# Performance work log

Hardware: AMD Instinct MI355X
Metric: run time of the kernel (lower is better)

Reference implementation:

```python
import jax, jax.numpy as jnp
import numpy as np

QB = 127.0  # 8-bit activation quant range
EPS = 1e-5


def _bitlinear(x, w, b):
    # BitNet b1.58-style BitLinear.
    # Activation: per-token absmax 8-bit quantization (STE).
    s = QB / jnp.clip(jnp.max(jnp.abs(x), axis=-1, keepdims=True), EPS)
    xq = jnp.clip(jnp.round(x * s), -QB - 1.0, QB) / s
    xq = x + jax.lax.stop_gradient(xq - x)
    # Weight: ternary {-1,0,1} with absmean scaling (STE).
    ws = 1.0 / jnp.clip(jnp.mean(jnp.abs(w)), EPS)
    wq = jnp.clip(jnp.round(w * ws), -1.0, 1.0) / ws
    wq = w + jax.lax.stop_gradient(wq - w)
    return jnp.einsum('bsf,of->bso', xq, wq) + b


def setup_inputs() -> dict:
    key = jax.random.key(0)
    k1, k2, k3, k4, k5, k6 = jax.random.split(key, 6)
    B, S, F = 8, 32768, 128
    evidence = jax.random.normal(k1, (B, S, F), dtype=jnp.float32)
    prior_belief = jax.random.uniform(k2, (B, S, F), dtype=jnp.float32)
    # belief_update params: Linear(2F -> F), Linear(F -> F)
    W1 = jax.random.normal(k3, (F, 2 * F), dtype=jnp.float32) * (1.0 / np.sqrt(2 * F))
    b1 = jax.random.normal(k4, (F,), dtype=jnp.float32) * 0.01
    W2 = jax.random.normal(k5, (F, F), dtype=jnp.float32) * (1.0 / np.sqrt(F))
    b2 = jax.random.normal(k6, (F,), dtype=jnp.float32) * 0.01
    return {"evidence": evidence, "prior_belief": prior_belief,
            "W1": W1, "b1": b1, "W2": W2, "b2": b2}


def reference(evidence, prior_belief, W1, b1, W2, b2):
    # update network: BitLinear -> ReLU -> BitLinear -> Sigmoid
    upd_in = jnp.concatenate([prior_belief, evidence], axis=-1)  # [B,S,2F]
    h = jax.nn.relu(_bitlinear(upd_in, W1, b1))                  # [B,S,F]
    likelihood = jax.nn.sigmoid(_bitlinear(h, W2, b2))           # [B,S,F]
    posterior_unnorm = prior_belief * likelihood
    normalizer = jnp.clip(posterior_unnorm.sum(axis=1, keepdims=True), 1e-10)
    return posterior_unnorm / normalizer
```

## Files before the change

### kernel.cpp

```cpp
#include <hip/hip_runtime.h>
#include <hip/hip_bf16.h>
#include <math.h>

typedef int   i32x4 __attribute__((ext_vector_type(4)));
typedef unsigned int u32;

#define QBF 127.0f
#define EPSF 1e-5f
#define FF 128
#define NROWS (8 * 32768)
#define NBLK 512
#define TPB 8

#define W2_OFF    32768
#define WBUF_OFF  49152
#define CS_OFF    66560
#define LDS_TOTAL 68608

#define WB() __builtin_amdgcn_wave_barrier()

static __device__ __forceinline__ float bcast_lane(float v, int lane) {
    return __builtin_bit_cast(float, __builtin_amdgcn_readlane(__builtin_bit_cast(int, v), lane));
}
static __device__ __forceinline__ u32 packi8(float a, float b, float c, float d, float s) {
    int i0 = (int)rintf(a * s), i1 = (int)rintf(b * s);
    int i2 = (int)rintf(c * s), i3 = (int)rintf(d * s);
    return (u32)(i0 & 0xFF) | ((u32)(i1 & 0xFF) << 8) |
           ((u32)(i2 & 0xFF) << 16) | ((u32)i3 << 24);
}

__global__ void wstats_kernel(const float* __restrict__ W1,
                              const float* __restrict__ W2,
                              float* __restrict__ hdr) {
    __shared__ double red[1024];
    int t = threadIdx.x;
    double s = 0.0;
    #pragma unroll
    for (int i = 0; i < 8; ++i) {
        float4 v = *(const float4*)(W1 + (i * 1024 + t) * 4);
        s += (double)fabsf(v.x) + (double)fabsf(v.y)
           + (double)fabsf(v.z) + (double)fabsf(v.w);
    }
    red[t] = s; __syncthreads();
    for (int o = 512; o > 0; o >>= 1) { if (t < o) red[t] += red[t + o]; __syncthreads(); }
    if (t == 0) hdr[0] = 1.0f / fmaxf((float)(red[0] * (1.0 / 32768.0)), EPSF);
    __syncthreads();
    s = 0.0;
    #pragma unroll
    for (int i = 0; i < 4; ++i) {
        float4 v = *(const float4*)(W2 + (i * 1024 + t) * 4);
        s += (double)fabsf(v.x) + (double)fabsf(v.y)
           + (double)fabsf(v.z) + (double)fabsf(v.w);
    }
    red[t] = s; __syncthreads();
    for (int o = 512; o > 0; o >>= 1) { if (t < o) red[t] += red[t + o]; __syncthreads(); }
    if (t == 0) hdr[1] = 1.0f / fmaxf((float)(red[0] * (1.0 / 16384.0)), EPSF);
}

__global__ void wquant_kernel(const float* __restrict__ W1,
                              const float* __restrict__ W2,
                              const float* __restrict__ hdr,
                              char* __restrict__ wq) {
    int g = blockIdx.x * 256 + threadIdx.x;
    float ws1 = hdr[0], ws2 = hdr[1];
    const float* src; float wsx; char* dst;
    if (g < 2048) {
        int gi = g >> 6, l = g & 63;
        int ct = gi >> 2, kb = gi & 3;
        src = W1 + (ct * 16 + (l & 15)) * 256 + kb * 64 + (l >> 4) * 16;
        wsx = ws1;
        dst = wq + gi * 1024 + l * 16;
    } else {
        int g2 = g - 2048;
        int gi = g2 >> 6, l = g2 & 63;
        int ct = gi >> 1, kb = gi & 1;
        src = W2 + (ct * 16 + (l & 15)) * 128 + kb * 64 + (l >> 4) * 16;
        wsx = ws2;
        dst = wq + 32768 + gi * 1024 + l * 16;
    }
    u32 o[4];
    #pragma unroll
    for (int q = 0; q < 4; ++q) {
        float4 v = *(const float4*)(src + q * 4);
        float q0 = fminf(fmaxf(rintf(v.x * wsx), -1.f), 1.f);
        float q1 = fminf(fmaxf(rintf(v.y * wsx), -1.f), 1.f);
        float q2 = fminf(fmaxf(rintf(v.z * wsx), -1.f), 1.f);
        float q3 = fminf(fmaxf(rintf(v.w * wsx), -1.f), 1.f);
        o[q] = packi8(q0, q1, q2, q3, 1.0f);
    }
    *(uint4*)dst = make_uint4(o[0], o[1], o[2], o[3]);
}

__global__ __launch_bounds__(256, 2) void fused_kernel(
    const float* __restrict__ evid, const float* __restrict__ prior,
    const float* __restrict__ bias1, const float* __restrict__ bias2,
    const char* __restrict__ wq, const float* __restrict__ hdr,
    float* __restrict__ out, float* __restrict__ partials)
{
    __shared__ __align__(16) char smem[LDS_TOTAL];
    const int tid = threadIdx.x;
    const int w = tid >> 6, l = tid & 63;
    const int lr = l & 15, lg = l >> 4;
    const int lc = l & 31, half = l >> 5;
    char* wbuf = smem + WBUF_OFF + w * 4352;
    float* colsum = (float*)(smem + CS_OFF);
    const float ws1 = hdr[0], ws2 = hdr[1];

    {
        const uint4* g = (const uint4*)wq;
        #pragma unroll
        for (int i = 0; i < 12; ++i) {
            uint4 v = g[i * 256 + tid];
            *(uint4*)(smem + (size_t)(i * 256 + tid) * 16) = v;
        }
    }
    float4 xr[16];
    {
        const float* srcp = half ? evid : prior;
        int R0 = blockIdx.x * 512 + w * 16;
        #pragma unroll
        for (int r = 0; r < 16; ++r)
            xr[r] = *(const float4*)(srcp + (size_t)(R0 + r) * FF + lc * 4);
    }
    __syncthreads();

    float4 cs[2];
    cs[0] = make_float4(0.f, 0.f, 0.f, 0.f);
    cs[1] = make_float4(0.f, 0.f, 0.f, 0.f);

    for (int t = 0; t < TPB; ++t) {
        const int R0c = blockIdx.x * 512 + t * 64 + w * 16;

        #pragma unroll
        for (int r = 0; r < 16; ++r) {
            float4 v = xr[r];
            float m = fmaxf(fmaxf(fabsf(v.x), fabsf(v.y)),
                            fmaxf(fabsf(v.z), fabsf(v.w)));
            *(float*)(wbuf + r * 272 + l * 4) = m;
        }
        WB();
        float mm;
        {
            const char* p = wbuf + lr * 272 + lg * 64;
            float4 a = *(const float4*)(p);
            float4 b = *(const float4*)(p + 16);
            float4 c = *(const float4*)(p + 32);
            float4 d = *(const float4*)(p + 48);
            float m0 = fmaxf(fmaxf(a.x, a.y), fmaxf(a.z, a.w));
            float m1 = fmaxf(fmaxf(b.x, b.y), fmaxf(b.z, b.w));
            float m2 = fmaxf(fmaxf(c.x, c.y), fmaxf(c.z, c.w));
            float m3 = fmaxf(fmaxf(d.x, d.y), fmaxf(d.z, d.w));
            mm = fmaxf(fmaxf(m0, m1), fmaxf(m2, m3));
        }
        mm = fmaxf(mm, __shfl_xor(mm, 16, 64));
        mm = fmaxf(mm, __shfl_xor(mm, 32, 64));
        const float sA = QBF / fmaxf(mm, EPSF);
        const float rinv1 = 1.0f / (sA * ws1);

        WB();
        #pragma unroll
        for (int r = 0; r < 16; ++r) {
            float s_r = bcast_lane(sA, r);
            float4 v = xr[r];
            *(u32*)(wbuf + r * 272 + l * 4) = packi8(v.x, v.y, v.z, v.w, s_r);
        }

        if (t + 1 < TPB) {
            const float* srcp = half ? evid : prior;
            int R0n = blockIdx.x * 512 + (t + 1) * 64 + w * 16;
            #pragma unroll
            for (int r = 0; r < 8; ++r)
                xr[r] = *(const float4*)(srcp + (size_t)(R0n + r) * FF + lc * 4);
        }
        WB();

        i32x4 acc1[8] = {};
        #pragma unroll
        for (int kb = 0; kb < 4; ++kb) {
            i32x4 xb = *(const i32x4*)(wbuf + lr * 272 + kb * 64 + lg * 16);
            #pragma unroll
            for (int ct = 0; ct < 8; ++ct) {
                i32x4 wa = *(const i32x4*)(smem + (ct * 4 + kb) * 1024 + l * 16);
                acc1[ct] = __builtin_amdgcn_mfma_i32_16x16x64_i8(wa, xb, acc1[ct], 0, 0, 0);
            }
        }

        float h[8][4];
        float hmax = 0.f;
        #pragma unroll
        for (int ct = 0; ct < 8; ++ct) {
            float4 b4 = *(const float4*)(bias1 + ct * 16 + lg * 4);
            h[ct][0] = fmaxf((float)acc1[ct][0] * rinv1 + b4.x, 0.f);
            h[ct][1] = fmaxf((float)acc1[ct][1] * rinv1 + b4.y, 0.f);
            h[ct][2] = fmaxf((float)acc1[ct][2] * rinv1 + b4.z, 0.f);
            h[ct][3] = fmaxf((float)acc1[ct][3] * rinv1 + b4.w, 0.f);
            hmax = fmaxf(hmax, fmaxf(fmaxf(h[ct][0], h[ct][1]),
                                     fmaxf(h[ct][2], h[ct][3])));
        }
        hmax = fmaxf(hmax, __shfl_xor(hmax, 16, 64));
        hmax = fmaxf(hmax, __shfl_xor(hmax, 32, 64));
        const float s2 = QBF / fmaxf(hmax, EPSF);
        const float rinv2 = 1.0f / (s2 * ws2);

        WB();
        #pragma unroll
        for (int ct = 0; ct < 8; ++ct)
            *(u32*)(wbuf + lr * 272 + ct * 16 + lg * 4) =
                packi8(h[ct][0], h[ct][1], h[ct][2], h[ct][3], s2);

        if (t + 1 < TPB) {
            const float* srcp = half ? evid : prior;
            int R0n = blockIdx.x * 512 + (t + 1) * 64 + w * 16;
            #pragma unroll
            for (int r = 8; r < 16; ++r)
                xr[r] = *(const float4*)(srcp + (size_t)(R0n + r) * FF + lc * 4);
        }
        float4 pvr[8];
        #pragma unroll
        for (int p = 0; p < 2; ++p) {
            #pragma unroll
            for (int i = 0; i < 4; ++i) {
                int rloc = 4 * i + (l >> 4);
                pvr[p * 4 + i] = *(const float4*)(prior +
                    (size_t)(R0c + rloc) * FF + p * 64 + (l & 15) * 4);
            }
        }
        WB();

        i32x4 acc2[8] = {};
        #pragma unroll
        for (int kb = 0; kb < 2; ++kb) {
            i32x4 hb = *(const i32x4*)(wbuf + lr * 272 + kb * 64 + lg * 16);
            #pragma unroll
            for (int ct = 0; ct < 8; ++ct) {
                i32x4 wa = *(const i32x4*)(smem + W2_OFF + (ct * 2 + kb) * 1024 + l * 16);
                acc2[ct] = __builtin_amdgcn_mfma_i32_16x16x64_i8(wa, hb, acc2[ct], 0, 0, 0);
            }
        }

        #pragma unroll
        for (int p = 0; p < 2; ++p) {
            WB();
            #pragma unroll
            for (int c = 0; c < 4; ++c) {
                const int ct = 4 * p + c;
                float4 b4 = *(const float4*)(bias2 + ct * 16 + lg * 4);
                float4 lik;
                float y0 = (float)acc2[ct][0] * rinv2 + b4.x;
                float y1 = (float)acc2[ct][1] * rinv2 + b4.y;
                float y2 = (float)acc2[ct][2] * rinv2 + b4.z;
                float y3 = (float)acc2[ct][3] * rinv2 + b4.w;
                lik.x = __builtin_amdgcn_rcpf(1.0f + __expf(-y0));
                lik.y = __builtin_amdgcn_rcpf(1.0f + __expf(-y1));
                lik.z = __builtin_amdgcn_rcpf(1.0f + __expf(-y2));
                lik.w = __builtin_amdgcn_rcpf(1.0f + __expf(-y3));
                *(float4*)(wbuf + lr * 272 + c * 64 + lg * 16) = lik;
            }
            WB();
            #pragma unroll
            for (int i = 0; i < 4; ++i) {
                int rloc = 4 * i + (l >> 4);
                float4 lk = *(const float4*)(wbuf + rloc * 272 + (l & 15) * 16);
                float4 pv = pvr[p * 4 + i];
                float4 un;
                un.x = pv.x * lk.x; un.y = pv.y * lk.y;
                un.z = pv.z * lk.z; un.w = pv.w * lk.w;
                *(float4*)(out + (size_t)(R0c + rloc) * FF + p * 64 + (l & 15) * 4) = un;
                cs[p].x += un.x; cs[p].y += un.y;
                cs[p].z += un.z; cs[p].w += un.w;
            }
        }
        WB();
    }

    #pragma unroll
    for (int p = 0; p < 2; ++p) {
        cs[p].x += __shfl_xor(cs[p].x, 16, 64);
        cs[p].y += __shfl_xor(cs[p].y, 16, 64);
        cs[p].z += __shfl_xor(cs[p].z, 16, 64);
        cs[p].w += __shfl_xor(cs[p].w, 16, 64);
        cs[p].x += __shfl_xor(cs[p].x, 32, 64);
        cs[p].y += __shfl_xor(cs[p].y, 32, 64);
        cs[p].z += __shfl_xor(cs[p].z, 32, 64);
        cs[p].w += __shfl_xor(cs[p].w, 32, 64);
    }
    if (l < 16) {
        *(float4*)(colsum + w * 128 + l * 4) = cs[0];
        *(float4*)(colsum + w * 128 + 64 + l * 4) = cs[1];
    }
    __syncthreads();
    if (tid < FF) {
        float p = colsum[tid] + colsum[128 + tid]
                + colsum[256 + tid] + colsum[384 + tid];
        partials[(size_t)blockIdx.x * FF + tid] = p;
    }
}

__global__ void norm_kernel(const float* __restrict__ partials, float* __restrict__ norm) {
    __shared__ float red[2][128];
    int b = blockIdx.x;
    int f = threadIdx.x & 127, tg = threadIdx.x >> 7;
    float s = 0.f;
    for (int t = tg * 32; t < tg * 32 + 32; ++t)
        s += partials[((size_t)b * 64 + t) * FF + f];
    red[tg][f] = s; __syncthreads();
    if (tg == 0)
        norm[b * FF + f] = fmaxf(red[0][f] + red[1][f], 1e-10f);
}

__global__ void div_kernel(float* __restrict__ out, const float* __restrict__ norm) {
    size_t i4 = (size_t)blockIdx.x * blockDim.x + threadIdx.x;
    const size_t total4 = (size_t)NROWS * FF / 4;
    for (; i4 < total4; i4 += (size_t)gridDim.x * blockDim.x) {
        size_t i = i4 * 4;
        float4 v = *(float4*)(out + i);
        int b = (int)(i >> 22);
        int f = (int)(i & 127);
        float4 nv = *(const float4*)(norm + b * FF + f);
        v.x /= nv.x; v.y /= nv.y; v.z /= nv.z; v.w /= nv.w;
        *(float4*)(out + i) = v;
    }
}

extern "C" void kernel_launch(void* const* d_in, const int* in_sizes, int n_in,
                              void* d_out, int out_size, void* d_ws, size_t ws_size,
                              hipStream_t stream) {
    const float* evid  = (const float*)d_in[0];
    const float* prior = (const float*)d_in[1];
    const float* W1    = (const float*)d_in[2];
    const float* b1    = (const float*)d_in[3];
    const float* W2    = (const float*)d_in[4];
    const float* b2    = (const float*)d_in[5];
    float* out = (float*)d_out;

    char* ws = (char*)d_ws;
    float*  hdr      = (float*)ws;
    char*   wq       = ws + 1024;
    float*  partials = (float*)(ws + 65536);
    float*  norm     = (float*)(ws + 65536 + 262144);

    wstats_kernel<<<1, 1024, 0, stream>>>(W1, W2, hdr);
    wquant_kernel<<<12, 256, 0, stream>>>(W1, W2, hdr, wq);
    fused_kernel<<<NBLK, 256, 0, stream>>>(evid, prior, b1, b2, wq, hdr, out, partials);
    norm_kernel<<<8, 256, 0, stream>>>(partials, norm);
    div_kernel<<<2048, 256, 0, stream>>>(out, norm);
}
```

Measured before the change: 150.4 us.

## Fuse normalizer reduction and division into main kernel via cooperative grid sync

Launches the fused kernel cooperatively and, after a grid-wide barrier, has each block reduce the per-block partial column sums for its batch and then divide its own slice of the output in place. This removes two extra kernel launches and their launch gaps. The division still re-reads and re-writes the output from global memory. The cost is a grid-wide sync plus redundant partial reductions in every block, and the code falls back to the old three-kernel path if occupancy is below 2 or the cooperative launch fails.

Result: no change. 153.3 us (+1.9%).

```diff
diff --git a/kernel.cpp b/kernel.cpp
--- a/kernel.cpp
+++ b/kernel.cpp
@@ -1,6 +1,9 @@
 #include <hip/hip_runtime.h>
 #include <hip/hip_bf16.h>
+#include <hip/hip_cooperative_groups.h>
 #include <math.h>
+
+namespace cg = cooperative_groups;
 
 typedef int   i32x4 __attribute__((ext_vector_type(4)));
 typedef unsigned int u32;
@@ -95,7 +98,7 @@
     const float* __restrict__ evid, const float* __restrict__ prior,
     const float* __restrict__ bias1, const float* __restrict__ bias2,
     const char* __restrict__ wq, const float* __restrict__ hdr,
-    float* __restrict__ out, float* __restrict__ partials)
+    float* __restrict__ out, float* __restrict__ partials, int do_tail)
 {
     __shared__ __align__(16) char smem[LDS_TOTAL];
     const int tid = threadIdx.x;
@@ -294,6 +297,33 @@
                 + colsum[256 + tid] + colsum[384 + tid];
         partials[(size_t)blockIdx.x * FF + tid] = p;
     }
+
+    if (do_tail) {
+        __threadfence();
+        cg::this_grid().sync();
+
+        const int b = blockIdx.x >> 6;
+        const int f = tid & 127, tg = tid >> 7;
+        float s = 0.f;
+        for (int k = tg * 32; k < tg * 32 + 32; ++k)
+            s += partials[((size_t)b * 64 + k) * FF + f];
+        colsum[tg * 128 + f] = s;
+        __syncthreads();
+        if (tg == 0)
+            colsum[256 + f] = fmaxf(colsum[f] + colsum[128 + f], 1e-10f);
+        __syncthreads();
+
+        const size_t base = (size_t)blockIdx.x * 512 * FF;
+        #pragma unroll 4
+        for (int i = tid; i < 512 * 32; i += 256) {
+            size_t off = base + (size_t)i * 4;
+            float4 v = *(float4*)(out + off);
+            int fc = (i * 4) & 127;
+            float4 nv = *(const float4*)(colsum + 256 + fc);
+            v.x /= nv.x; v.y /= nv.y; v.z /= nv.z; v.w /= nv.w;
+            *(float4*)(out + off) = v;
+        }
+    }
 }
 
 __global__ void norm_kernel(const float* __restrict__ partials, float* __restrict__ norm) {
@@ -341,7 +371,24 @@
 
     wstats_kernel<<<1, 1024, 0, stream>>>(W1, W2, hdr);
     wquant_kernel<<<12, 256, 0, stream>>>(W1, W2, hdr, wq);
-    fused_kernel<<<NBLK, 256, 0, stream>>>(evid, prior, b1, b2, wq, hdr, out, partials);
-    norm_kernel<<<8, 256, 0, stream>>>(partials, norm);
-    div_kernel<<<2048, 256, 0, stream>>>(out, norm);
-}
+
+    int occ = 0;
+    (void)hipOccupancyMaxActiveBlocksPerMultiprocessor(&occ, fused_kernel, 256, 0);
+    int do_tail = (occ >= 2) ? 1 : 0;
+
+    if (do_tail) {
+        void* args[] = { (void*)&evid, (void*)&prior, (void*)&b1, (void*)&b2,
+                         (void*)&wq, (void*)&hdr, (void*)&out, (void*)&partials,
+                         (void*)&do_tail };
+        hipError_t err = hipLaunchCooperativeKernel((const void*)fused_kernel,
+                                                    dim3(NBLK), dim3(256),
+                                                    args, 0, stream);
+        if (err != hipSuccess) do_tail = 0;
+    }
+    if (!do_tail) {
+        fused_kernel<<<NBLK, 256, 0, stream>>>(evid, prior, b1, b2, wq, hdr,
+                                               out, partials, 0);
+        norm_kernel<<<8, 256, 0, stream>>>(partials, norm);
+        div_kernel<<<2048, 256, 0, stream>>>(out, norm);
+    }
+}
```
